# Performance work log

Measured on AMD Instinct MI355X. Metric: run time of the kernel, lower is better.

## Reference

```python
import jax, jax.numpy as jnp
import numpy as np

LN_EPS = 1e-5

def _layernorm(x, g, b):
    mu = jnp.mean(x, axis=-1, keepdims=True)
    var = jnp.var(x, axis=-1, keepdims=True)
    return (x - mu) * jax.lax.rsqrt(var + LN_EPS) * g + b

def setup_inputs() -> dict:
    key = jax.random.key(0)
    B, S, D, H = 2, 2048, 1024, 16
    dh = D // H          # 64
    r = 48               # r_attn = int(0.75*min(D,dh))
    r_out = 768          # int(0.75*D)
    I = 4 * D            # GPT-2 MLP inner dim
    r_mlp = 512          # int(0.5*min(D,I))
    ks = jax.random.split(key, 24)
    sc = lambda *sh: 0.02
    inp = {
        'hidden_states': jax.random.normal(ks[0], (B, S, D), jnp.float32),
        'ln1_g': jnp.ones((D,), jnp.float32), 'ln1_b': jnp.zeros((D,), jnp.float32),
        'ln2_g': jnp.ones((D,), jnp.float32), 'ln2_b': jnp.zeros((D,), jnp.float32),
        'q_U': jax.random.normal(ks[1], (D, H, r), jnp.float32) * 0.02,
        'q_V': jax.random.normal(ks[2], (H, r, dh), jnp.float32) * 0.02,
        'q_b': jax.random.normal(ks[3], (H, dh), jnp.float32) * 0.02,
        'k_U': jax.random.normal(ks[4], (D, H, r), jnp.float32) * 0.02,
        'k_V': jax.random.normal(ks[5], (H, r, dh), jnp.float32) * 0.02,
        'k_b': jax.random.normal(ks[6], (H, dh), jnp.float32) * 0.02,
        'v_U': jax.random.normal(ks[7], (D, H, r), jnp.float32) * 0.02,
        'v_V': jax.random.normal(ks[8], (H, r, dh), jnp.float32) * 0.02,
        'v_b': jax.random.normal(ks[9], (H, dh), jnp.float32) * 0.02,
        'out_U': jax.random.normal(ks[10], (D, r_out), jnp.float32) * 0.02,
        'out_V': jax.random.normal(ks[11], (r_out, D), jnp.float32) * 0.02,
        'out_b': jnp.zeros((D,), jnp.float32),
        'fc1_U': jax.random.normal(ks[12], (D, r_mlp), jnp.float32) * 0.02,
        'fc1_V': jax.random.normal(ks[13], (r_mlp, I), jnp.float32) * 0.02,
        'fc1_b': jnp.zeros((I,), jnp.float32),
        'fc2_U': jax.random.normal(ks[14], (I, r_mlp), jnp.float32) * 0.02,
        'fc2_V': jax.random.normal(ks[15], (r_mlp, D), jnp.float32) * 0.02,
        'fc2_b': jnp.zeros((D,), jnp.float32),
    }
    return inp

def reference(hidden_states, ln1_g, ln1_b, ln2_g, ln2_b,
              q_U, q_V, q_b, k_U, k_V, k_b, v_U, v_V, v_b,
              out_U, out_V, out_b, fc1_U, fc1_V, fc1_b, fc2_U, fc2_V, fc2_b):
    B, S, D = hidden_states.shape
    H, dh = q_V.shape[0], q_V.shape[2]
    x = _layernorm(hidden_states, ln1_g, ln1_b)
    # low-rank per-head projections (latent P then reconstruct)
    Q = jnp.einsum('bsd,dhr,hre->bhse', x, q_U, q_V) + q_b[None, :, None, :]
    Pk = jnp.einsum('bsd,dhr->bhsr', x, k_U)
    Pv = jnp.einsum('bsd,dhr->bhsr', x, v_U)
    K = jnp.einsum('bhsr,hrd->bhsd', Pk, k_V) + k_b[None, :, None, :]
    V = jnp.einsum('bhsr,hrd->bhsd', Pv, v_V) + v_b[None, :, None, :]
    # causal scaled dot-product attention
    scale = 1.0 / jnp.sqrt(jnp.asarray(dh, x.dtype))
    scores = jnp.einsum('bhse,bhte->bhst', Q, K) * scale
    causal = jnp.tril(jnp.ones((S, S), bool))
    scores = jnp.where(causal[None, None], scores, jnp.asarray(-1e9, scores.dtype))
    attn = jax.nn.softmax(scores, axis=-1)
    ctx = jnp.einsum('bhst,bhtd->bhsd', attn, V)          # [B,H,S,dh]
    ctx = ctx.transpose(0, 2, 1, 3).reshape(B, S, D)
    attn_out = (ctx @ out_U) @ out_V + out_b
    h = hidden_states + attn_out
    # low-rank MLP with GPT-2 gelu (tanh approx)
    x2 = _layernorm(h, ln2_g, ln2_b)
    hmid = jax.nn.gelu((x2 @ fc1_U) @ fc1_V + fc1_b, approximate=True)
    mlp_out = (hmid @ fc2_U) @ fc2_V + fc2_b
    return h + mlp_out
```

## Files before the change

### kernel.cpp

```cpp
#include <hip/hip_runtime.h>
#include <hip/hip_bf16.h>

typedef float f32x4 __attribute__((ext_vector_type(4)));
typedef __bf16 bf16x8 __attribute__((ext_vector_type(8)));
typedef unsigned short u16x8 __attribute__((ext_vector_type(8)));
typedef unsigned short u16x4 __attribute__((ext_vector_type(4)));

#define QSCALE 0.180336881f

__device__ __forceinline__ unsigned short f2bf(float f) {
  union { float f; unsigned int u; } v; v.f = f;
  return (unsigned short)((v.u + 0x7FFFu + ((v.u >> 16) & 1u)) >> 16);
}

__device__ __forceinline__ f32x4 mfma16(bf16x8 a, bf16x8 b, f32x4 c) {
  return __builtin_amdgcn_mfma_f32_16x16x32_bf16(a, b, c, 0, 0, 0);
}

__device__ __forceinline__ void gload16(const unsigned short* g, unsigned short* l) {
  __builtin_amdgcn_global_load_lds(
      (const __attribute__((address_space(1))) void*)g,
      (__attribute__((address_space(3))) void*)l, 16, 0, 0);
}


__global__ void concat_bias_k(const float* __restrict__ qb, const float* __restrict__ kb,
                              const float* __restrict__ vb, float* __restrict__ out) {
  const int i = blockIdx.x * 256 + threadIdx.x;
  if (i >= 3072) return;
  const float* s = (i < 1024) ? qb : (i < 2048 ? kb : vb);
  out[i] = s[i & 1023] * (i < 1024 ? QSCALE : 1.0f);
}

__global__ void tcvt_k(const float* __restrict__ in, unsigned short* __restrict__ out,
                       int R, int C) {
  __shared__ float tile[32][33];
  const int x = blockIdx.x * 32 + threadIdx.x;
  const int y0 = blockIdx.y * 32;
#pragma unroll
  for (int i = 0; i < 32; i += 8)
    tile[threadIdx.y + i][threadIdx.x] = in[(size_t)(y0 + threadIdx.y + i) * C + x];
  __syncthreads();
  const int ox = y0 + threadIdx.x;
  const int oy0 = blockIdx.x * 32;
#pragma unroll
  for (int i = 0; i < 32; i += 8)
    out[(size_t)(oy0 + threadIdx.y + i) * R + ox] = f2bf(tile[threadIdx.x][threadIdx.y + i]);
}

__global__ void cvt_k(const float* __restrict__ in, unsigned short* __restrict__ out, int n) {
  const int i = (blockIdx.x * 256 + threadIdx.x) * 4;
  if (i >= n) return;
  const f32x4 v = *(const f32x4*)(in + i);
  u16x4 o;
#pragma unroll
  for (int k = 0; k < 4; ++k) o[k] = f2bf(v[k]);
  *(u16x4*)(out + i) = o;
}

__global__ void vtr_k(const unsigned short* __restrict__ QKV, unsigned short* __restrict__ VT) {
  __shared__ unsigned short tile[32][33];
  const int bh = blockIdx.z, b = bh >> 4, h = bh & 15;
  const int s0 = blockIdx.x * 32, d0 = blockIdx.y * 32;
  const unsigned short* src = QKV + (size_t)b * 2048 * 3072 + 2048 + h * 64;
#pragma unroll
  for (int i = 0; i < 32; i += 8)
    tile[threadIdx.y + i][threadIdx.x] = src[(size_t)(s0 + threadIdx.y + i) * 3072 + d0 + threadIdx.x];
  __syncthreads();
  unsigned short* dst = VT + (size_t)bh * 64 * 2048;
#pragma unroll
  for (int i = 0; i < 32; i += 8)
    dst[(size_t)(d0 + threadIdx.y + i) * 2048 + s0 + threadIdx.x] = tile[threadIdx.x][threadIdx.y + i];
}

__global__ __launch_bounds__(256) void wqkv_pre_k(
    const float* __restrict__ qU, const float* __restrict__ qV,
    const float* __restrict__ kU, const float* __restrict__ kV,
    const float* __restrict__ vU, const float* __restrict__ vV,
    unsigned short* __restrict__ WT) {
  __shared__ float Us[64][48];
  __shared__ float Vs[48][64];
  const int m = blockIdx.y >> 4, h = blockIdx.y & 15;
  const int d0 = blockIdx.x * 64;
  const float* U = (m == 0) ? qU : (m == 1 ? kU : vU);
  const float* V = (m == 0) ? qV : (m == 1 ? kV : vV);
  const float qs = (m == 0) ? QSCALE : 1.0f;
  const int t = threadIdx.x;
  for (int idx = t; idx < 64 * 48; idx += 256) {
    const int d = idx / 48, r = idx - d * 48;
    Us[d][r] = U[(size_t)(d0 + d) * 768 + h * 48 + r];
  }
  for (int idx = t; idx < 48 * 64; idx += 256) {
    const int r = idx >> 6, e = idx & 63;
    Vs[r][e] = V[(h * 48 + r) * 64 + e];
  }
  __syncthreads();
  const int e = t & 63, dg = t >> 6;
  for (int j = 0; j < 16; ++j) {
    const int d = dg * 16 + j;
    float s = 0.f;
#pragma unroll
    for (int r = 0; r < 48; ++r) s = fmaf(Us[d][r], Vs[r][e], s);
    WT[(size_t)(m * 1024 + h * 64 + e) * 1024 + d0 + d] = f2bf(s * qs);
  }
}

__global__ __launch_bounds__(256) void ln_k(
    const float* __restrict__ in, const float* __restrict__ gw,
    const float* __restrict__ bw, unsigned short* __restrict__ out) {
  const int row = blockIdx.x, t = threadIdx.x;
  const f32x4 v = *(const f32x4*)(in + (size_t)row * 1024 + t * 4);
  float s = v[0] + v[1] + v[2] + v[3];
  float ss = v[0] * v[0] + v[1] * v[1] + v[2] * v[2] + v[3] * v[3];
#pragma unroll
  for (int off = 1; off < 64; off <<= 1) {
    s += __shfl_xor(s, off);
    ss += __shfl_xor(ss, off);
  }
  __shared__ float red[8];
  if ((t & 63) == 0) { red[(t >> 6) * 2] = s; red[(t >> 6) * 2 + 1] = ss; }
  __syncthreads();
  s = red[0] + red[2] + red[4] + red[6];
  ss = red[1] + red[3] + red[5] + red[7];
  const float mean = s * (1.0f / 1024.0f);
  const float rstd = rsqrtf(ss * (1.0f / 1024.0f) - mean * mean + 1e-5f);
  const f32x4 g4 = *(const f32x4*)(gw + t * 4);
  const f32x4 b4 = *(const f32x4*)(bw + t * 4);
  u16x4 o;
#pragma unroll
  for (int i = 0; i < 4; ++i) o[i] = f2bf((v[i] - mean) * rstd * g4[i] + b4[i]);
  *(u16x4*)(out + (size_t)row * 1024 + t * 4) = o;
}

__device__ __forceinline__ void xcd_swz(int& bx, int& by, int nx, int ny) {
  const int nwg = nx * ny;
  if ((nwg & 7) == 0) {
    const int d = by * nx + bx;
    const int k = (d & 7) * (nwg >> 3) + (d >> 3);
    bx = k % nx;
    by = k / nx;
  }
}

template <int BM, int BN, int EPI, int OUTBF>
__global__ __launch_bounds__(256) void gemm_k(
    const unsigned short* __restrict__ A, const unsigned short* __restrict__ Bt,
    const float* __restrict__ bias, const float* __restrict__ resid,
    void* __restrict__ Cout, int M, int N, int K) {
  constexpr int MI = BM / 32;
  constexpr int FN = BN / 32;
  __shared__ unsigned short As[2][BM * 32];
  __shared__ unsigned short Bs[2][BN * 32];
  int bxi = blockIdx.x, byi = blockIdx.y;
  xcd_swz(bxi, byi, gridDim.x, gridDim.y);
  const int t = threadIdx.x;
  const int lane = t & 63, wid = t >> 6;
  const int m0 = byi * BM, n0 = bxi * BN;
  const int wm = (wid >> 1) * (BM / 2), wn = (wid & 1) * (BN / 2);
  const int fr = lane & 15, fg = (lane >> 4) * 8;

  f32x4 acc[MI][FN];
#pragma unroll
  for (int i = 0; i < MI; ++i)
#pragma unroll
    for (int j = 0; j < FN; ++j) acc[i][j] = (f32x4){0.f, 0.f, 0.f, 0.f};

  const unsigned short* Ag0 = A + (size_t)(m0 + (t >> 2)) * K + (t & 3) * 8;
  const unsigned short* Ag1 = A + (size_t)(m0 + 64 + (t >> 2)) * K + (t & 3) * 8;
  const unsigned short* Bg0 = Bt + (size_t)(n0 + (t >> 2)) * K + (t & 3) * 8;
  const unsigned short* Bg1 = Bt + (size_t)(n0 + 64 + (t >> 2)) * K + (t & 3) * 8;
  const int l0 = t * 8;

#define GEMM_STAGE(buf, ke)                                   \
  {                                                           \
    gload16(Ag0 + (ke), &As[buf][l0]);                        \
    if (BM == 128) gload16(Ag1 + (ke), &As[buf][l0 + 2048]);  \
    gload16(Bg0 + (ke), &Bs[buf][l0]);                        \
    if (BN == 128) gload16(Bg1 + (ke), &Bs[buf][l0 + 2048]);  \
  }

  const int nk = K >> 5;
  GEMM_STAGE(0, 0);

  for (int kt = 0; kt < nk; ++kt) {
    const int cur = kt & 1;
    __syncthreads();
    if (kt + 1 < nk) GEMM_STAGE(cur ^ 1, (kt + 1) * 32);
    bf16x8 af[MI], bfr[FN];
#pragma unroll
    for (int i = 0; i < MI; ++i) af[i] = *(const bf16x8*)&As[cur][(wm + i * 16 + fr) * 32 + fg];
#pragma unroll
    for (int j = 0; j < FN; ++j) bfr[j] = *(const bf16x8*)&Bs[cur][(wn + j * 16 + fr) * 32 + fg];
#pragma unroll
    for (int i = 0; i < MI; ++i)
#pragma unroll
      for (int j = 0; j < FN; ++j) acc[i][j] = mfma16(af[i], bfr[j], acc[i][j]);
  }
#undef GEMM_STAGE

#pragma unroll
  for (int j = 0; j < FN; ++j) {
    const int col = n0 + wn + j * 16 + fr;
    const float bval = (EPI >= 1) ? bias[col] : 0.0f;
#pragma unroll
    for (int i = 0; i < MI; ++i) {
#pragma unroll
      for (int r = 0; r < 4; ++r) {
        const int row = m0 + wm + i * 16 + ((lane >> 4) << 2) + r;
        float v = acc[i][j][r] + bval;
        if (EPI == 2) {
          const float z = 0.7978845608028654f * (v + 0.044715f * v * v * v);
          v = v - v / (__expf(2.0f * z) + 1.0f);
        }
        if (EPI == 3) v += resid[(size_t)row * N + col];
        if (OUTBF)
          ((unsigned short*)Cout)[(size_t)row * N + col] = f2bf(v);
        else
          ((float*)Cout)[(size_t)row * N + col] = v;
      }
    }
  }
}

__global__ __launch_bounds__(256) void attn_k(
    const unsigned short* __restrict__ QKV, const unsigned short* __restrict__ VT,
    unsigned short* __restrict__ ctx) {
  __shared__ unsigned short Ks[2][64 * 64];
  __shared__ unsigned short Vs[2][64 * 64];
  __shared__ __bf16 Ps[4][16][64];
  int bxi = blockIdx.x, byi = blockIdx.y;
  xcd_swz(bxi, byi, 32, 32);
  const int qt = 31 - bxi, bh = byi;
  const int nt = qt + 1;
  const int b = bh >> 4, h = bh & 15;
  const int t = threadIdx.x, lane = t & 63, w = t >> 6;
  const int g = lane >> 4, c = lane & 15;
  const int cks = c & 7;
  const int q0 = qt * 64;
  const size_t base = (size_t)b * 2048 * 3072;

  const int r0 = t >> 2;
  const int ch0 = (t & 3) * 2;
  const int lw0 = r0 * 64 + ((ch0 ^ (r0 & 7)) * 8);
  const int lw1 = r0 * 64 + (((ch0 + 1) ^ (r0 & 7)) * 8);
  const unsigned short* Kg = QKV + base + 1024 + h * 64 + (size_t)r0 * 3072 + ch0 * 8;
  const unsigned short* Vg = VT + ((size_t)bh * 64 + r0) * 2048 + ch0 * 8;

  const int kro0 = (g ^ cks) * 8, kro1 = ((4 + g) ^ cks) * 8;

  bf16x8 onef;
#pragma unroll
  for (int i = 0; i < 8; ++i) onef[i] = (__bf16)1.0f;

  const unsigned short* qp = QKV + base + (size_t)(q0 + w * 16 + c) * 3072 + h * 64 + g * 8;
  const bf16x8 qf0 = *(const bf16x8*)qp;
  const bf16x8 qf1 = *(const bf16x8*)(qp + 32);

  f32x4 o[4];
#pragma unroll
  for (int d = 0; d < 4; ++d) o[d] = (f32x4){0.f, 0.f, 0.f, 0.f};
  f32x4 ol = (f32x4){0.f, 0.f, 0.f, 0.f};
  float mrow[4];
#pragma unroll
  for (int r = 0; r < 4; ++r) mrow[r] = -1e30f;

  u16x8 kr0, kr1, vr0, vr1;

#define ATTN_LOAD(kt_)                                      \
  {                                                         \
    const size_t ko = (size_t)(kt_) * 64 * 3072;            \
    const int vo = (kt_) * 64;                              \
    kr0 = *(const u16x8*)(Kg + ko);                         \
    kr1 = *(const u16x8*)(Kg + ko + 8);                     \
    vr0 = *(const u16x8*)(Vg + vo);                         \
    vr1 = *(const u16x8*)(Vg + vo + 8);                     \
  }
#define ATTN_WRITE(buf)                                     \
  {                                                         \
    *(u16x8*)&Ks[buf][lw0] = kr0;                           \
    *(u16x8*)&Ks[buf][lw1] = kr1;                           \
    *(u16x8*)&Vs[buf][lw0] = vr0;                           \
    *(u16x8*)&Vs[buf][lw1] = vr1;                           \
  }

  ATTN_LOAD(0);
  ATTN_WRITE(0);
  if (nt > 1) ATTN_LOAD(1);
  __syncthreads();

  for (int j = 0; j < nt; ++j) {
    const int cur = j & 1;

    f32x4 s4[4];
    __builtin_amdgcn_s_setprio(1);
#pragma unroll
    for (int t16 = 0; t16 < 4; ++t16) {
      const int krow = (t16 * 16 + c) * 64;
      const bf16x8 kf0 = *(const bf16x8*)&Ks[cur][krow + kro0];
      const bf16x8 kf1 = *(const bf16x8*)&Ks[cur][krow + kro1];
      f32x4 a = (f32x4){0.f, 0.f, 0.f, 0.f};
      a = mfma16(qf0, kf0, a);
      a = mfma16(qf1, kf1, a);
      s4[t16] = a;
    }
    __builtin_amdgcn_s_setprio(0);
    if (j == qt) {
      const int qbase = q0 + w * 16 + g * 4;
      const int kbase = j * 64 + c;
#pragma unroll
      for (int t16 = 0; t16 < 4; ++t16)
#pragma unroll
        for (int r = 0; r < 4; ++r)
          if (kbase + t16 * 16 > qbase + r) s4[t16][r] = -1e30f;
    }
    float mx[4];
#pragma unroll
    for (int r = 0; r < 4; ++r)
      mx[r] = fmaxf(fmaxf(s4[0][r], s4[1][r]), fmaxf(s4[2][r], s4[3][r]));
#pragma unroll
    for (int off = 1; off < 16; off <<= 1)
#pragma unroll
      for (int r = 0; r < 4; ++r) mx[r] = fmaxf(mx[r], __shfl_xor(mx[r], off));
    float fac[4];
#pragma unroll
    for (int r = 0; r < 4; ++r) {
      const float mn = fmaxf(mrow[r], mx[r]);
      fac[r] = exp2f(mrow[r] - mn);
      mrow[r] = mn;
    }
#pragma unroll
    for (int t16 = 0; t16 < 4; ++t16)
#pragma unroll
      for (int r = 0; r < 4; ++r) {
        const int q = g * 4 + r;
        const int col = (((t16 * 2 + (c >> 3)) ^ (q & 7)) * 8) + cks;
        Ps[w][q][col] = (__bf16)exp2f(s4[t16][r] - mrow[r]);
      }
#pragma unroll
    for (int d = 0; d < 4; ++d)
#pragma unroll
      for (int r = 0; r < 4; ++r) o[d][r] *= fac[r];
#pragma unroll
    for (int r = 0; r < 4; ++r) ol[r] *= fac[r];
    __builtin_amdgcn_s_setprio(1);
#pragma unroll
    for (int ks = 0; ks < 2; ++ks) {
      const bf16x8 pf = *(const bf16x8*)&Ps[w][c][ks ? kro1 : kro0];
#pragma unroll
      for (int d = 0; d < 4; ++d) {
        const bf16x8 vf = *(const bf16x8*)&Vs[cur][(d * 16 + c) * 64 + (ks ? kro1 : kro0)];
        o[d] = mfma16(pf, vf, o[d]);
      }
      ol = mfma16(pf, onef, ol);
    }
    __builtin_amdgcn_s_setprio(0);

    if (j + 1 < nt) {
      __syncthreads();
      ATTN_WRITE(cur ^ 1);
      if (j + 2 < nt) ATTN_LOAD(j + 2);
      __syncthreads();
    }
  }
#pragma unroll
  for (int d = 0; d < 4; ++d)
#pragma unroll
    for (int r = 0; r < 4; ++r) {
      const float v = o[d][r] / ol[r];
      ctx[(size_t)(b * 2048 + q0 + w * 16 + g * 4 + r) * 1024 + h * 64 + d * 16 + c] = f2bf(v);
    }
#undef ATTN_LOAD
#undef ATTN_WRITE
}


extern "C" void kernel_launch(void* const* d_in, const int* in_sizes, int n_in,
                              void* d_out, int out_size, void* d_ws, size_t ws_size,
                              hipStream_t stream) {
  const float* hidden = (const float*)d_in[0];
  const float* ln1g = (const float*)d_in[1];
  const float* ln1b = (const float*)d_in[2];
  const float* ln2g = (const float*)d_in[3];
  const float* ln2b = (const float*)d_in[4];
  const float* qU = (const float*)d_in[5];
  const float* qV = (const float*)d_in[6];
  const float* qb = (const float*)d_in[7];
  const float* kU = (const float*)d_in[8];
  const float* kV = (const float*)d_in[9];
  const float* kb = (const float*)d_in[10];
  const float* vU = (const float*)d_in[11];
  const float* vV = (const float*)d_in[12];
  const float* vb = (const float*)d_in[13];
  const float* outU = (const float*)d_in[14];
  const float* outV = (const float*)d_in[15];
  const float* outb = (const float*)d_in[16];
  const float* fc1U = (const float*)d_in[17];
  const float* fc1V = (const float*)d_in[18];
  const float* fc1b = (const float*)d_in[19];
  const float* fc2U = (const float*)d_in[20];
  const float* fc2V = (const float*)d_in[21];
  const float* fc2b = (const float*)d_in[22];
  float* out = (float*)d_out;

  char* p = (char*)d_ws;
  unsigned short* x1x2 = (unsigned short*)p; p += (size_t)4096 * 1024 * 2;
  unsigned short* WqT_t1 = (unsigned short*)p; p += (size_t)3072 * 1024 * 2;
  float* bqkv = (float*)p; p += 3072 * 4;
  char* bigA = p; p += (size_t)4096 * 3072 * 2 + (size_t)4096 * 1024 * 2;
  unsigned short* QKV = (unsigned short*)bigA;
  unsigned short* ctxb = (unsigned short*)(bigA + (size_t)4096 * 3072 * 2);
  unsigned short* hmid = (unsigned short*)bigA;
  char* wo = p; p += (size_t)1024 * 768 * 2 * 2 + (size_t)1024 * 1024 * 2;
  unsigned short* outUb = (unsigned short*)wo;
  unsigned short* outVT = (unsigned short*)(wo + (size_t)1024 * 768 * 2);
  unsigned short* WoutT = (unsigned short*)(wo + (size_t)1024 * 768 * 2 * 2);
  unsigned short* t2 = (unsigned short*)wo;
  float* hbuf = (float*)p; p += (size_t)4096 * 1024 * 4;
  unsigned short* VT = (unsigned short*)hbuf;
  unsigned short* fc1UT = (unsigned short*)p; p += (size_t)512 * 1024 * 2;
  unsigned short* fc1VT = (unsigned short*)p; p += (size_t)4096 * 512 * 2;
  unsigned short* fc2UT = (unsigned short*)p; p += (size_t)512 * 4096 * 2;
  unsigned short* fc2VT = (unsigned short*)p; p += (size_t)1024 * 512 * 2;

  const dim3 b256(256);
  const dim3 tb(32, 8);

  concat_bias_k<<<12, b256, 0, stream>>>(qb, kb, vb, bqkv);
  wqkv_pre_k<<<dim3(16, 48), b256, 0, stream>>>(qU, qV, kU, kV, vU, vV, WqT_t1);
  tcvt_k<<<dim3(32, 24), tb, 0, stream>>>(outV, outVT, 768, 1024);
  cvt_k<<<768, b256, 0, stream>>>(outU, outUb, 1024 * 768);
  tcvt_k<<<dim3(16, 32), tb, 0, stream>>>(fc1U, fc1UT, 1024, 512);
  tcvt_k<<<dim3(128, 16), tb, 0, stream>>>(fc1V, fc1VT, 512, 4096);
  tcvt_k<<<dim3(16, 128), tb, 0, stream>>>(fc2U, fc2UT, 4096, 512);
  tcvt_k<<<dim3(32, 16), tb, 0, stream>>>(fc2V, fc2VT, 512, 1024);

  ln_k<<<4096, b256, 0, stream>>>(hidden, ln1g, ln1b, x1x2);
  gemm_k<128, 128, 1, 1><<<dim3(24, 32), b256, 0, stream>>>(x1x2, WqT_t1, bqkv, nullptr, QKV, 4096, 3072, 1024);
  vtr_k<<<dim3(64, 2, 32), tb, 0, stream>>>(QKV, VT);
  gemm_k<128, 128, 0, 1><<<dim3(8, 8), b256, 0, stream>>>(outVT, outUb, nullptr, nullptr, WoutT, 1024, 1024, 768);
  attn_k<<<dim3(32, 32), b256, 0, stream>>>(QKV, VT, ctxb);
  gemm_k<64, 128, 3, 0><<<dim3(8, 64), b256, 0, stream>>>(ctxb, WoutT, outb, hidden, hbuf, 4096, 1024, 1024);

  ln_k<<<4096, b256, 0, stream>>>(hbuf, ln2g, ln2b, x1x2);
  gemm_k<64, 64, 0, 1><<<dim3(8, 64), b256, 0, stream>>>(x1x2, fc1UT, nullptr, nullptr, WqT_t1, 4096, 512, 1024);
  gemm_k<128, 128, 2, 1><<<dim3(32, 32), b256, 0, stream>>>(WqT_t1, fc1VT, fc1b, nullptr, hmid, 4096, 4096, 512);
  gemm_k<64, 64, 0, 1><<<dim3(8, 64), b256, 0, stream>>>(hmid, fc2UT, nullptr, nullptr, t2, 4096, 512, 4096);
  gemm_k<64, 128, 3, 0><<<dim3(8, 64), b256, 0, stream>>>(t2, fc2VT, fc2b, hbuf, out, 4096, 1024, 512);
}
```

Baseline: 313.7 us.

## Widen attention blocks to 128 query rows with 8 waves and transposed score MFMA

The attention kernel now uses 512-thread blocks covering 128 query rows, so each K/V tile staged in shared memory is reused by eight waves instead of four, and the grid is halved. Query tiles are reordered per head pair to balance causal work. The QK^T MFMA operands are swapped so each lane holds one query row; the row max then needs only two cross-lane shuffles and P is written with vector stores. Waves whose rows lie entirely before a key tile skip it, which adds branching and a lane shuffle to redistribute the rescale factors.

```diff
diff --git a/kernel.cpp b/kernel.cpp
--- a/kernel.cpp
+++ b/kernel.cpp
@@ -3,6 +3,7 @@
 
 typedef float f32x4 __attribute__((ext_vector_type(4)));
 typedef __bf16 bf16x8 __attribute__((ext_vector_type(8)));
+typedef __bf16 bf16x4 __attribute__((ext_vector_type(4)));
 typedef unsigned short u16x8 __attribute__((ext_vector_type(8)));
 typedef unsigned short u16x4 __attribute__((ext_vector_type(4)));
 
@@ -222,27 +223,25 @@
   }
 }
 
-__global__ __launch_bounds__(256) void attn_k(
+__global__ __launch_bounds__(512) void attn_k(
     const unsigned short* __restrict__ QKV, const unsigned short* __restrict__ VT,
     unsigned short* __restrict__ ctx) {
   __shared__ unsigned short Ks[2][64 * 64];
   __shared__ unsigned short Vs[2][64 * 64];
-  __shared__ __bf16 Ps[4][16][64];
+  __shared__ unsigned short Ps[8][16 * 64];
   int bxi = blockIdx.x, byi = blockIdx.y;
-  xcd_swz(bxi, byi, 32, 32);
-  const int qt = 31 - bxi, bh = byi;
-  const int nt = qt + 1;
-  const int b = bh >> 4, h = bh & 15;
+  xcd_swz(bxi, byi, 16, 32);
+  const int qi = ((byi >> 1) & 1) ? (15 - bxi) : bxi;
+  const int bh = byi, b = bh >> 4, h = bh & 15;
+  const int nt = 2 * qi + 2;
+  const int q0b = qi * 128;
   const int t = threadIdx.x, lane = t & 63, w = t >> 6;
   const int g = lane >> 4, c = lane & 15;
   const int cks = c & 7;
-  const int q0 = qt * 64;
   const size_t base = (size_t)b * 2048 * 3072;
 
-  const int r0 = t >> 2;
-  const int ch0 = (t & 3) * 2;
-  const int lw0 = r0 * 64 + ((ch0 ^ (r0 & 7)) * 8);
-  const int lw1 = r0 * 64 + (((ch0 + 1) ^ (r0 & 7)) * 8);
+  const int r0 = t >> 3, ch0 = t & 7;
+  const int lw = r0 * 64 + ((ch0 ^ (r0 & 7)) * 8);
   const unsigned short* Kg = QKV + base + 1024 + h * 64 + (size_t)r0 * 3072 + ch0 * 8;
   const unsigned short* Vg = VT + ((size_t)bh * 64 + r0) * 2048 + ch0 * 8;
 
@@ -252,7 +251,8 @@
 #pragma unroll
   for (int i = 0; i < 8; ++i) onef[i] = (__bf16)1.0f;
 
-  const unsigned short* qp = QKV + base + (size_t)(q0 + w * 16 + c) * 3072 + h * 64 + g * 8;
+  const int qrow = q0b + w * 16 + c;
+  const unsigned short* qp = QKV + base + (size_t)qrow * 3072 + h * 64 + g * 8;
   const bf16x8 qf0 = *(const bf16x8*)qp;
   const bf16x8 qf1 = *(const bf16x8*)(qp + 32);
 
@@ -260,27 +260,18 @@
 #pragma unroll
   for (int d = 0; d < 4; ++d) o[d] = (f32x4){0.f, 0.f, 0.f, 0.f};
   f32x4 ol = (f32x4){0.f, 0.f, 0.f, 0.f};
-  float mrow[4];
-#pragma unroll
-  for (int r = 0; r < 4; ++r) mrow[r] = -1e30f;
-
-  u16x8 kr0, kr1, vr0, vr1;
-
-#define ATTN_LOAD(kt_)                                      \
-  {                                                         \
-    const size_t ko = (size_t)(kt_) * 64 * 3072;            \
-    const int vo = (kt_) * 64;                              \
-    kr0 = *(const u16x8*)(Kg + ko);                         \
-    kr1 = *(const u16x8*)(Kg + ko + 8);                     \
-    vr0 = *(const u16x8*)(Vg + vo);                         \
-    vr1 = *(const u16x8*)(Vg + vo + 8);                     \
-  }
-#define ATTN_WRITE(buf)                                     \
-  {                                                         \
-    *(u16x8*)&Ks[buf][lw0] = kr0;                           \
-    *(u16x8*)&Ks[buf][lw1] = kr1;                           \
-    *(u16x8*)&Vs[buf][lw0] = vr0;                           \
-    *(u16x8*)&Vs[buf][lw1] = vr1;                           \
+  float mrow = -1e30f;
+
+  u16x8 kr, vr;
+#define ATTN_LOAD(kt_)                                        \
+  {                                                           \
+    kr = *(const u16x8*)(Kg + (size_t)(kt_) * 64 * 3072);     \
+    vr = *(const u16x8*)(Vg + (kt_) * 64);                    \
+  }
+#define ATTN_WRITE(buf)                                       \
+  {                                                           \
+    *(u16x8*)&Ks[buf][lw] = kr;                               \
+    *(u16x8*)&Vs[buf][lw] = vr;                               \
   }
 
   ATTN_LOAD(0);
@@ -288,72 +279,74 @@
   if (nt > 1) ATTN_LOAD(1);
   __syncthreads();
 
+  const int fsrc = g * 20;
+
   for (int j = 0; j < nt; ++j) {
     const int cur = j & 1;
-
-    f32x4 s4[4];
-    __builtin_amdgcn_s_setprio(1);
-#pragma unroll
-    for (int t16 = 0; t16 < 4; ++t16) {
-      const int krow = (t16 * 16 + c) * 64;
-      const bf16x8 kf0 = *(const bf16x8*)&Ks[cur][krow + kro0];
-      const bf16x8 kf1 = *(const bf16x8*)&Ks[cur][krow + kro1];
-      f32x4 a = (f32x4){0.f, 0.f, 0.f, 0.f};
-      a = mfma16(qf0, kf0, a);
-      a = mfma16(qf1, kf1, a);
-      s4[t16] = a;
+    const int kbase = j * 64;
+    const bool active = (kbase <= q0b + w * 16 + 15);
+
+    if (active) {
+      f32x4 s4[4];
+      __builtin_amdgcn_s_setprio(1);
+#pragma unroll
+      for (int t16 = 0; t16 < 4; ++t16) {
+        const int krow = (t16 * 16 + c) * 64;
+        const bf16x8 kf0 = *(const bf16x8*)&Ks[cur][krow + kro0];
+        const bf16x8 kf1 = *(const bf16x8*)&Ks[cur][krow + kro1];
+        f32x4 a = (f32x4){0.f, 0.f, 0.f, 0.f};
+        a = mfma16(kf0, qf0, a);
+        a = mfma16(kf1, qf1, a);
+        s4[t16] = a;
+      }
+      __builtin_amdgcn_s_setprio(0);
+      if (kbase + 63 > qrow) {
+#pragma unroll
+        for (int t16 = 0; t16 < 4; ++t16)
+#pragma unroll
+          for (int r = 0; r < 4; ++r)
+            if (kbase + t16 * 16 + 4 * g + r > qrow) s4[t16][r] = -1e30f;
+      }
+      float mx = s4[0][0];
+#pragma unroll
+      for (int t16 = 0; t16 < 4; ++t16)
+#pragma unroll
+        for (int r = 0; r < 4; ++r) mx = fmaxf(mx, s4[t16][r]);
+      mx = fmaxf(mx, __shfl_xor(mx, 16));
+      mx = fmaxf(mx, __shfl_xor(mx, 32));
+      const float mn = fmaxf(mrow, mx);
+      const float fac = exp2f(mrow - mn);
+      mrow = mn;
+#pragma unroll
+      for (int t16 = 0; t16 < 4; ++t16) {
+        bf16x4 pw;
+#pragma unroll
+        for (int r = 0; r < 4; ++r) pw[r] = (__bf16)exp2f(s4[t16][r] - mrow);
+        *(bf16x4*)&Ps[w][c * 64 + (((2 * t16 + (g >> 1)) ^ cks) * 8) + (g & 1) * 4] = pw;
+      }
+      float fo[4];
+#pragma unroll
+      for (int r = 0; r < 4; ++r) fo[r] = __shfl(fac, fsrc + r);
+#pragma unroll
+      for (int d = 0; d < 4; ++d)
+#pragma unroll
+        for (int r = 0; r < 4; ++r) o[d][r] *= fo[r];
+#pragma unroll
+      for (int r = 0; r < 4; ++r) ol[r] *= fo[r];
+      __builtin_amdgcn_s_setprio(1);
+#pragma unroll
+      for (int ks = 0; ks < 2; ++ks) {
+        const int po = ((ks * 4 + g) ^ cks) * 8;
+        const bf16x8 pf = *(const bf16x8*)&Ps[w][c * 64 + po];
+#pragma unroll
+        for (int d = 0; d < 4; ++d) {
+          const bf16x8 vf = *(const bf16x8*)&Vs[cur][(d * 16 + c) * 64 + po];
+          o[d] = mfma16(pf, vf, o[d]);
+        }
+        ol = mfma16(pf, onef, ol);
+      }
+      __builtin_amdgcn_s_setprio(0);
     }
-    __builtin_amdgcn_s_setprio(0);
-    if (j == qt) {
-      const int qbase = q0 + w * 16 + g * 4;
-      const int kbase = j * 64 + c;
-#pragma unroll
-      for (int t16 = 0; t16 < 4; ++t16)
-#pragma unroll
-        for (int r = 0; r < 4; ++r)
-          if (kbase + t16 * 16 > qbase + r) s4[t16][r] = -1e30f;
-    }
-    float mx[4];
-#pragma unroll
-    for (int r = 0; r < 4; ++r)
-      mx[r] = fmaxf(fmaxf(s4[0][r], s4[1][r]), fmaxf(s4[2][r], s4[3][r]));
-#pragma unroll
-    for (int off = 1; off < 16; off <<= 1)
-#pragma unroll
-      for (int r = 0; r < 4; ++r) mx[r] = fmaxf(mx[r], __shfl_xor(mx[r], off));
-    float fac[4];
-#pragma unroll
-    for (int r = 0; r < 4; ++r) {
-      const float mn = fmaxf(mrow[r], mx[r]);
-      fac[r] = exp2f(mrow[r] - mn);
-      mrow[r] = mn;
-    }
-#pragma unroll
-    for (int t16 = 0; t16 < 4; ++t16)
-#pragma unroll
-      for (int r = 0; r < 4; ++r) {
-        const int q = g * 4 + r;
-        const int col = (((t16 * 2 + (c >> 3)) ^ (q & 7)) * 8) + cks;
-        Ps[w][q][col] = (__bf16)exp2f(s4[t16][r] - mrow[r]);
-      }
-#pragma unroll
-    for (int d = 0; d < 4; ++d)
-#pragma unroll
-      for (int r = 0; r < 4; ++r) o[d][r] *= fac[r];
-#pragma unroll
-    for (int r = 0; r < 4; ++r) ol[r] *= fac[r];
-    __builtin_amdgcn_s_setprio(1);
-#pragma unroll
-    for (int ks = 0; ks < 2; ++ks) {
-      const bf16x8 pf = *(const bf16x8*)&Ps[w][c][ks ? kro1 : kro0];
-#pragma unroll
-      for (int d = 0; d < 4; ++d) {
-        const bf16x8 vf = *(const bf16x8*)&Vs[cur][(d * 16 + c) * 64 + (ks ? kro1 : kro0)];
-        o[d] = mfma16(pf, vf, o[d]);
-      }
-      ol = mfma16(pf, onef, ol);
-    }
-    __builtin_amdgcn_s_setprio(0);
 
     if (j + 1 < nt) {
       __syncthreads();
@@ -367,7 +360,7 @@
 #pragma unroll
     for (int r = 0; r < 4; ++r) {
       const float v = o[d][r] / ol[r];
-      ctx[(size_t)(b * 2048 + q0 + w * 16 + g * 4 + r) * 1024 + h * 64 + d * 16 + c] = f2bf(v);
+      ctx[(size_t)(b * 2048 + q0b + w * 16 + g * 4 + r) * 1024 + h * 64 + d * 16 + c] = f2bf(v);
     }
 #undef ATTN_LOAD
 #undef ATTN_WRITE
@@ -438,7 +431,7 @@
   gemm_k<128, 128, 1, 1><<<dim3(24, 32), b256, 0, stream>>>(x1x2, WqT_t1, bqkv, nullptr, QKV, 4096, 3072, 1024);
   vtr_k<<<dim3(64, 2, 32), tb, 0, stream>>>(QKV, VT);
   gemm_k<128, 128, 0, 1><<<dim3(8, 8), b256, 0, stream>>>(outVT, outUb, nullptr, nullptr, WoutT, 1024, 1024, 768);
-  attn_k<<<dim3(32, 32), b256, 0, stream>>>(QKV, VT, ctxb);
+  attn_k<<<dim3(16, 32), dim3(512), 0, stream>>>(QKV, VT, ctxb);
   gemm_k<64, 128, 3, 0><<<dim3(8, 64), b256, 0, stream>>>(ctxb, WoutT, outb, hidden, hbuf, 4096, 1024, 1024);
 
   ln_k<<<4096, b256, 0, stream>>>(hbuf, ln2g, ln2b, x1x2);
```

Result: faster. 291.4 us (-7.1%).
